# Performance work log

Hardware: AMD Instinct MI355X
Metric: run time of the kernel (lower is better)

## Reference

```python
import jax, jax.numpy as jnp
import numpy as np

EPS_PD = 1e-6   # torch F.pairwise_distance default eps (added to the difference)
EPS_CS = 1e-8   # torch cosine_similarity default eps (norm clamp)


def _similarity(f1, f2, f3):
    # f1, f2, f3: (B, D)
    w1 = 1.0 / (1.0 + jnp.sqrt(jnp.sum((f1 - f2 + EPS_PD) ** 2, axis=-1, keepdims=True)))
    w2 = 1.0 / (1.0 + jnp.sqrt(jnp.sum((f1 - f3 + EPS_PD) ** 2, axis=-1, keepdims=True)))
    n1 = jnp.maximum(jnp.sqrt(jnp.sum(f1 * f1, axis=-1, keepdims=True)), EPS_CS)
    n2 = jnp.maximum(jnp.sqrt(jnp.sum(f2 * f2, axis=-1, keepdims=True)), EPS_CS)
    n3 = jnp.maximum(jnp.sqrt(jnp.sum(f3 * f3, axis=-1, keepdims=True)), EPS_CS)
    w3 = 0.5 + 0.5 * (jnp.sum(f1 * f2, axis=-1, keepdims=True) / (n1 * n2))
    w4 = 0.5 + 0.5 * (jnp.sum(f1 * f3, axis=-1, keepdims=True) / (n1 * n3))
    return f1 + (w1 + w3) * f2 + (w2 + w4) * f3


def setup_inputs() -> dict:
    key = jax.random.key(0)
    k1, k2 = jax.random.split(key)
    B, steps, D = 8192, 3, 2048
    feat_in = jax.random.normal(k1, (B * steps, D), dtype=jnp.float32)
    pos_embedding = jax.random.normal(k2, (1, steps, D), dtype=jnp.float32)
    return {"feat_in": feat_in, "pos_embedding": pos_embedding}


def reference(feat_in, pos_embedding):
    steps = pos_embedding.shape[1]   # 3
    D = pos_embedding.shape[2]
    B = feat_in.shape[0] // steps
    x = feat_in.reshape(B, steps, D) + pos_embedding   # (B, 3, D)
    f1, f2, f3 = x[:, 0], x[:, 1], x[:, 2]
    o1 = _similarity(f1, f2, f3)
    o2 = _similarity(f2, f1, f3)
    o3 = _similarity(f3, f1, f2)
    out = jnp.stack((o1, o2, o3), axis=1)              # (B, 3, D)
    return out.reshape(B * steps, D)
```

## Files before the change

### kernel.cpp

```cpp
#include <hip/hip_runtime.h>


constexpr int D   = 2048;
constexpr int TPB = 256;
constexpr int RPB = TPB / 64;
constexpr int NC  = D / (64 * 4);
constexpr float EPS_PD = 1e-6f;
constexpr float EPS_CS = 1e-8f;

using fvec4 = __attribute__((ext_vector_type(4))) float;

__global__ __launch_bounds__(TPB) void feat_corr_kernel(
    const float* __restrict__ feat,
    const float* __restrict__ pos,
    float* __restrict__ out,
    int B)
{
    const int wave = threadIdx.x >> 6;
    const int lane = threadIdx.x & 63;
    const int b    = blockIdx.x * RPB + wave;
    if (b >= B) return;

    const size_t row = (size_t)b * (3 * D);
    const fvec4* r1 = (const fvec4*)(feat + row);
    const fvec4* r2 = r1 + D / 4;
    const fvec4* r3 = r2 + D / 4;
    const fvec4* p1 = (const fvec4*)(pos);
    const fvec4* p2 = p1 + D / 4;
    const fvec4* p3 = p2 + D / 4;

    fvec4 x1[NC], x2[NC], x3[NC];
#pragma unroll
    for (int j = 0; j < NC; ++j) x1[j] = r1[j * 64 + lane];
#pragma unroll
    for (int j = 0; j < NC; ++j) x2[j] = r2[j * 64 + lane];
#pragma unroll
    for (int j = 0; j < NC; ++j) x3[j] = r3[j * 64 + lane];

#pragma unroll
    for (int j = 0; j < NC; ++j) {
        x1[j] += p1[j * 64 + lane];
        x2[j] += p2[j * 64 + lane];
        x3[j] += p3[j * 64 + lane];
    }

    float n1s = 0.f, n2s = 0.f, n3s = 0.f;
    float d12 = 0.f, d13 = 0.f, d23 = 0.f;
    float s1  = 0.f, s2  = 0.f, s3  = 0.f;
#pragma unroll
    for (int j = 0; j < NC; ++j) {
#pragma unroll
        for (int k = 0; k < 4; ++k) {
            const float u = x1[j][k], w = x2[j][k], z = x3[j][k];
            n1s = fmaf(u, u, n1s);
            n2s = fmaf(w, w, n2s);
            n3s = fmaf(z, z, n3s);
            d12 = fmaf(u, w, d12);
            d13 = fmaf(u, z, d13);
            d23 = fmaf(w, z, d23);
            s1 += u; s2 += w; s3 += z;
        }
    }

    float vals[9] = {n1s, n2s, n3s, d12, d13, d23, s1, s2, s3};
#pragma unroll
    for (int off = 1; off < 64; off <<= 1) {
#pragma unroll
        for (int k = 0; k < 9; ++k)
            vals[k] += __shfl_xor(vals[k], off, 64);
    }

    const float N1s = vals[0], N2s = vals[1], N3s = vals[2];
    const float D12 = vals[3], D13 = vals[4], D23 = vals[5];
    const float S1  = vals[6], S2  = vals[7], S3  = vals[8];

    const float n1 = fmaxf(sqrtf(N1s), EPS_CS);
    const float n2 = fmaxf(sqrtf(N2s), EPS_CS);
    const float n3 = fmaxf(sqrtf(N3s), EPS_CS);

    const float c12 = 0.5f + 0.5f * (D12 / (n1 * n2));
    const float c13 = 0.5f + 0.5f * (D13 / (n1 * n3));
    const float c23 = 0.5f + 0.5f * (D23 / (n2 * n3));

    const float sq12 = N1s + N2s - 2.f * D12;
    const float sq13 = N1s + N3s - 2.f * D13;
    const float sq23 = N2s + N3s - 2.f * D23;
    const float De2  = (float)D * EPS_PD * EPS_PD;

    auto wdist = [&](float sqd, float ssum) {
        return 1.0f / (1.0f + sqrtf(sqd + 2.f * EPS_PD * ssum + De2));
    };
    const float w12 = wdist(sq12, S1 - S2);
    const float w21 = wdist(sq12, S2 - S1);
    const float w13 = wdist(sq13, S1 - S3);
    const float w31 = wdist(sq13, S3 - S1);
    const float w23 = wdist(sq23, S2 - S3);
    const float w32 = wdist(sq23, S3 - S2);

    const float g1b = w12 + c12, g1c = w13 + c13;
    const float g2a = w21 + c12, g2c = w23 + c23;
    const float g3a = w31 + c13, g3b = w32 + c23;

    fvec4* o1 = (fvec4*)(out + row);
    fvec4* o2 = o1 + D / 4;
    fvec4* o3 = o2 + D / 4;
#pragma unroll
    for (int j = 0; j < NC; ++j) {
        const int idx = j * 64 + lane;
        fvec4 q1 = x1[j] + g1b * x2[j] + g1c * x3[j];
        fvec4 q2 = x2[j] + g2a * x1[j] + g2c * x3[j];
        fvec4 q3 = x3[j] + g3a * x1[j] + g3b * x2[j];
        __builtin_nontemporal_store(q1, o1 + idx);
        __builtin_nontemporal_store(q2, o2 + idx);
        __builtin_nontemporal_store(q3, o3 + idx);
    }
}

extern "C" void kernel_launch(void* const* d_in, const int* in_sizes, int n_in,
                              void* d_out, int out_size, void* d_ws, size_t ws_size,
                              hipStream_t stream) {
    const float* feat = (const float*)d_in[0];
    const float* pos  = (const float*)d_in[1];
    float* out        = (float*)d_out;
    const int B = in_sizes[0] / (3 * D * (int)sizeof(float));
    const int B_rows = in_sizes[0] / (3 * D);
    const int Buse   = (B_rows > 0) ? B_rows : B;
    const int grid   = (Buse + RPB - 1) / RPB;
    feat_corr_kernel<<<grid, TPB, 0, stream>>>(feat, pos, out, Buse);
}
```

Baseline: 340.6 us.

## Use persistent waves with double-buffered row prefetch and LDS-cached position embedding

Switches from one wave per row to a persistent grid capped at 512 blocks, where each wave strides over rows. It loads the next row into a second register buffer while the current row is processed, overlapping loads with compute and stores. The position embedding is staged into shared memory once per block rather than read from global memory for every row. Two full row buffers per thread raise register pressure sharply, which limits occupancy and risks spills. The capped grid may also leave some CUs underused.

Measured after the change: 362.4 us. 1.06x slower.

```diff
diff --git a/kernel.cpp b/kernel.cpp
--- a/kernel.cpp
+++ b/kernel.cpp
@@ -3,116 +3,144 @@
 
 constexpr int D   = 2048;
 constexpr int TPB = 256;
-constexpr int RPB = TPB / 64;
+constexpr int WPB = TPB / 64;
 constexpr int NC  = D / (64 * 4);
 constexpr float EPS_PD = 1e-6f;
 constexpr float EPS_CS = 1e-8f;
 
 using fvec4 = __attribute__((ext_vector_type(4))) float;
 
-__global__ __launch_bounds__(TPB) void feat_corr_kernel(
+__global__ __launch_bounds__(TPB, 2) void feat_corr_kernel(
     const float* __restrict__ feat,
     const float* __restrict__ pos,
     float* __restrict__ out,
-    int B)
+    int B, int NW)
 {
-    const int wave = threadIdx.x >> 6;
+    __shared__ float pshared[3 * D];
+    {
+        const fvec4* ps = (const fvec4*)pos;
+        fvec4*       pd = (fvec4*)pshared;
+        for (int i = threadIdx.x; i < 3 * D / 4; i += TPB)
+            pd[i] = ps[i];
+    }
+    __syncthreads();
+
     const int lane = threadIdx.x & 63;
-    const int b    = blockIdx.x * RPB + wave;
-    if (b >= B) return;
+    const int gw   = blockIdx.x * WPB + (threadIdx.x >> 6);
 
-    const size_t row = (size_t)b * (3 * D);
-    const fvec4* r1 = (const fvec4*)(feat + row);
-    const fvec4* r2 = r1 + D / 4;
-    const fvec4* r3 = r2 + D / 4;
-    const fvec4* p1 = (const fvec4*)(pos);
+    const fvec4* p1 = (const fvec4*)pshared;
     const fvec4* p2 = p1 + D / 4;
     const fvec4* p3 = p2 + D / 4;
 
-    fvec4 x1[NC], x2[NC], x3[NC];
+    fvec4 xA1[NC], xA2[NC], xA3[NC];
+    fvec4 xB1[NC], xB2[NC], xB3[NC];
+
+    auto load_row = [&](fvec4 (&x1)[NC], fvec4 (&x2)[NC], fvec4 (&x3)[NC], int b) {
+        const fvec4* r1 = (const fvec4*)(feat + (size_t)b * (3 * D));
+        const fvec4* r2 = r1 + D / 4;
+        const fvec4* r3 = r2 + D / 4;
 #pragma unroll
-    for (int j = 0; j < NC; ++j) x1[j] = r1[j * 64 + lane];
+        for (int j = 0; j < NC; ++j) x1[j] = r1[j * 64 + lane];
 #pragma unroll
-    for (int j = 0; j < NC; ++j) x2[j] = r2[j * 64 + lane];
+        for (int j = 0; j < NC; ++j) x2[j] = r2[j * 64 + lane];
 #pragma unroll
-    for (int j = 0; j < NC; ++j) x3[j] = r3[j * 64 + lane];
+        for (int j = 0; j < NC; ++j) x3[j] = r3[j * 64 + lane];
+    };
 
+    auto process_row = [&](fvec4 (&x1)[NC], fvec4 (&x2)[NC], fvec4 (&x3)[NC], int b) {
 #pragma unroll
-    for (int j = 0; j < NC; ++j) {
-        x1[j] += p1[j * 64 + lane];
-        x2[j] += p2[j * 64 + lane];
-        x3[j] += p3[j * 64 + lane];
-    }
+        for (int j = 0; j < NC; ++j) {
+            x1[j] += p1[j * 64 + lane];
+            x2[j] += p2[j * 64 + lane];
+            x3[j] += p3[j * 64 + lane];
+        }
 
-    float n1s = 0.f, n2s = 0.f, n3s = 0.f;
-    float d12 = 0.f, d13 = 0.f, d23 = 0.f;
-    float s1  = 0.f, s2  = 0.f, s3  = 0.f;
+        float n1s = 0.f, n2s = 0.f, n3s = 0.f;
+        float d12 = 0.f, d13 = 0.f, d23 = 0.f;
+        float s1  = 0.f, s2  = 0.f, s3  = 0.f;
 #pragma unroll
-    for (int j = 0; j < NC; ++j) {
+        for (int j = 0; j < NC; ++j) {
 #pragma unroll
-        for (int k = 0; k < 4; ++k) {
-            const float u = x1[j][k], w = x2[j][k], z = x3[j][k];
-            n1s = fmaf(u, u, n1s);
-            n2s = fmaf(w, w, n2s);
-            n3s = fmaf(z, z, n3s);
-            d12 = fmaf(u, w, d12);
-            d13 = fmaf(u, z, d13);
-            d23 = fmaf(w, z, d23);
-            s1 += u; s2 += w; s3 += z;
+            for (int k = 0; k < 4; ++k) {
+                const float u = x1[j][k], w = x2[j][k], z = x3[j][k];
+                n1s = fmaf(u, u, n1s);
+                n2s = fmaf(w, w, n2s);
+                n3s = fmaf(z, z, n3s);
+                d12 = fmaf(u, w, d12);
+                d13 = fmaf(u, z, d13);
+                d23 = fmaf(w, z, d23);
+                s1 += u; s2 += w; s3 += z;
+            }
         }
-    }
 
-    float vals[9] = {n1s, n2s, n3s, d12, d13, d23, s1, s2, s3};
+        float vals[9] = {n1s, n2s, n3s, d12, d13, d23, s1, s2, s3};
 #pragma unroll
-    for (int off = 1; off < 64; off <<= 1) {
+        for (int off = 1; off < 64; off <<= 1) {
 #pragma unroll
-        for (int k = 0; k < 9; ++k)
-            vals[k] += __shfl_xor(vals[k], off, 64);
-    }
+            for (int k = 0; k < 9; ++k)
+                vals[k] += __shfl_xor(vals[k], off, 64);
+        }
 
-    const float N1s = vals[0], N2s = vals[1], N3s = vals[2];
-    const float D12 = vals[3], D13 = vals[4], D23 = vals[5];
-    const float S1  = vals[6], S2  = vals[7], S3  = vals[8];
+        const float N1s = vals[0], N2s = vals[1], N3s = vals[2];
+        const float D12 = vals[3], D13 = vals[4], D23 = vals[5];
+        const float S1  = vals[6], S2  = vals[7], S3  = vals[8];
 
-    const float n1 = fmaxf(sqrtf(N1s), EPS_CS);
-    const float n2 = fmaxf(sqrtf(N2s), EPS_CS);
-    const float n3 = fmaxf(sqrtf(N3s), EPS_CS);
+        const float n1 = fmaxf(sqrtf(N1s), EPS_CS);
+        const float n2 = fmaxf(sqrtf(N2s), EPS_CS);
+        const float n3 = fmaxf(sqrtf(N3s), EPS_CS);
 
-    const float c12 = 0.5f + 0.5f * (D12 / (n1 * n2));
-    const float c13 = 0.5f + 0.5f * (D13 / (n1 * n3));
-    const float c23 = 0.5f + 0.5f * (D23 / (n2 * n3));
+        const float c12 = 0.5f + 0.5f * (D12 / (n1 * n2));
+        const float c13 = 0.5f + 0.5f * (D13 / (n1 * n3));
+        const float c23 = 0.5f + 0.5f * (D23 / (n2 * n3));
 
-    const float sq12 = N1s + N2s - 2.f * D12;
-    const float sq13 = N1s + N3s - 2.f * D13;
-    const float sq23 = N2s + N3s - 2.f * D23;
-    const float De2  = (float)D * EPS_PD * EPS_PD;
+        const float sq12 = N1s + N2s - 2.f * D12;
+        const float sq13 = N1s + N3s - 2.f * D13;
+        const float sq23 = N2s + N3s - 2.f * D23;
+        const float De2  = (float)D * EPS_PD * EPS_PD;
 
-    auto wdist = [&](float sqd, float ssum) {
-        return 1.0f / (1.0f + sqrtf(sqd + 2.f * EPS_PD * ssum + De2));
+        auto wdist = [&](float sqd, float ssum) {
+            return 1.0f / (1.0f + sqrtf(sqd + 2.f * EPS_PD * ssum + De2));
+        };
+        const float w12 = wdist(sq12, S1 - S2);
+        const float w21 = wdist(sq12, S2 - S1);
+        const float w13 = wdist(sq13, S1 - S3);
+        const float w31 = wdist(sq13, S3 - S1);
+        const float w23 = wdist(sq23, S2 - S3);
+        const float w32 = wdist(sq23, S3 - S2);
+
+        const float g1b = w12 + c12, g1c = w13 + c13;
+        const float g2a = w21 + c12, g2c = w23 + c23;
+        const float g3a = w31 + c13, g3b = w32 + c23;
+
+        const size_t row = (size_t)b * (3 * D);
+        fvec4* o1 = (fvec4*)(out + row);
+        fvec4* o2 = o1 + D / 4;
+        fvec4* o3 = o2 + D / 4;
+#pragma unroll
+        for (int j = 0; j < NC; ++j) {
+            const int idx = j * 64 + lane;
+            fvec4 q1 = x1[j] + g1b * x2[j] + g1c * x3[j];
+            fvec4 q2 = x2[j] + g2a * x1[j] + g2c * x3[j];
+            fvec4 q3 = x3[j] + g3a * x1[j] + g3b * x2[j];
+            __builtin_nontemporal_store(q1, o1 + idx);
+            __builtin_nontemporal_store(q2, o2 + idx);
+            __builtin_nontemporal_store(q3, o3 + idx);
+        }
     };
-    const float w12 = wdist(sq12, S1 - S2);
-    const float w21 = wdist(sq12, S2 - S1);
-    const float w13 = wdist(sq13, S1 - S3);
-    const float w31 = wdist(sq13, S3 - S1);
-    const float w23 = wdist(sq23, S2 - S3);
-    const float w32 = wdist(sq23, S3 - S2);
 
-    const float g1b = w12 + c12, g1c = w13 + c13;
-    const float g2a = w21 + c12, g2c = w23 + c23;
-    const float g3a = w31 + c13, g3b = w32 + c23;
-
-    fvec4* o1 = (fvec4*)(out + row);
-    fvec4* o2 = o1 + D / 4;
-    fvec4* o3 = o2 + D / 4;
-#pragma unroll
-    for (int j = 0; j < NC; ++j) {
-        const int idx = j * 64 + lane;
-        fvec4 q1 = x1[j] + g1b * x2[j] + g1c * x3[j];
-        fvec4 q2 = x2[j] + g2a * x1[j] + g2c * x3[j];
-        fvec4 q3 = x3[j] + g3a * x1[j] + g3b * x2[j];
-        __builtin_nontemporal_store(q1, o1 + idx);
-        __builtin_nontemporal_store(q2, o2 + idx);
-        __builtin_nontemporal_store(q3, o3 + idx);
+    int r = gw;
+    if (r >= B) return;
+    load_row(xA1, xA2, xA3, r);
+    while (true) {
+        const int rB = r + NW;
+        if (rB < B) load_row(xB1, xB2, xB3, rB);
+        process_row(xA1, xA2, xA3, r);
+        if (rB >= B) break;
+        const int rn = r + 2 * NW;
+        if (rn < B) load_row(xA1, xA2, xA3, rn);
+        process_row(xB1, xB2, xB3, rB);
+        if (rn >= B) break;
+        r = rn;
     }
 }
 
@@ -122,9 +150,9 @@
     const float* feat = (const float*)d_in[0];
     const float* pos  = (const float*)d_in[1];
     float* out        = (float*)d_out;
-    const int B = in_sizes[0] / (3 * D * (int)sizeof(float));
-    const int B_rows = in_sizes[0] / (3 * D);
-    const int Buse   = (B_rows > 0) ? B_rows : B;
-    const int grid   = (Buse + RPB - 1) / RPB;
-    feat_corr_kernel<<<grid, TPB, 0, stream>>>(feat, pos, out, Buse);
+    const int B = in_sizes[0] / (3 * D);
+    int blocks = (B + WPB - 1) / WPB;
+    if (blocks > 512) blocks = 512;
+    const int NW = blocks * WPB;
+    feat_corr_kernel<<<blocks, TPB, 0, stream>>>(feat, pos, out, B, NW);
 }
```

## Split into reduce and combine kernels with LDS-cached positional embedding

Applied to the files above, without the earlier changes.

Splits the single register-heavy kernel into two passes. The first computes the per-row coefficients into workspace, and the second re-reads the features and writes the combined output. Both stage the positional embedding in shared memory and use launch bounds that ask for higher occupancy. The per-row sums behind the epsilon term are also dropped, which simplifies the distance weights. The cost is a second full read of the 200MB input in exchange for lower register pressure, plus a small accuracy deviation from removing the eps*sum term.

New measurement: 446.7 us. 31.1% more time.

```diff
diff --git a/kernel.cpp b/kernel.cpp
--- a/kernel.cpp
+++ b/kernel.cpp
@@ -3,76 +3,68 @@
 
 constexpr int D   = 2048;
 constexpr int TPB = 256;
-constexpr int RPB = TPB / 64;
+constexpr int WPB = TPB / 64;
 constexpr int NC  = D / (64 * 4);
 constexpr float EPS_PD = 1e-6f;
 constexpr float EPS_CS = 1e-8f;
 
 using fvec4 = __attribute__((ext_vector_type(4))) float;
 
-__global__ __launch_bounds__(TPB) void feat_corr_kernel(
+__global__ __launch_bounds__(TPB, 6) void feat_corr_reduce(
     const float* __restrict__ feat,
     const float* __restrict__ pos,
-    float* __restrict__ out,
+    float* __restrict__ coef,
     int B)
 {
-    const int wave = threadIdx.x >> 6;
+    __shared__ float psh[3 * D];
+    {
+        const fvec4* ps = (const fvec4*)pos;
+        fvec4*       pd = (fvec4*)psh;
+        for (int i = threadIdx.x; i < 3 * D / 4; i += TPB) pd[i] = ps[i];
+    }
+    __syncthreads();
+
     const int lane = threadIdx.x & 63;
-    const int b    = blockIdx.x * RPB + wave;
+    const int b    = blockIdx.x * WPB + (threadIdx.x >> 6);
     if (b >= B) return;
 
-    const size_t row = (size_t)b * (3 * D);
-    const fvec4* r1 = (const fvec4*)(feat + row);
+    const fvec4* r1 = (const fvec4*)(feat + (size_t)b * (3 * D));
     const fvec4* r2 = r1 + D / 4;
     const fvec4* r3 = r2 + D / 4;
-    const fvec4* p1 = (const fvec4*)(pos);
+    const fvec4* p1 = (const fvec4*)psh;
     const fvec4* p2 = p1 + D / 4;
     const fvec4* p3 = p2 + D / 4;
 
-    fvec4 x1[NC], x2[NC], x3[NC];
-#pragma unroll
-    for (int j = 0; j < NC; ++j) x1[j] = r1[j * 64 + lane];
-#pragma unroll
-    for (int j = 0; j < NC; ++j) x2[j] = r2[j * 64 + lane];
-#pragma unroll
-    for (int j = 0; j < NC; ++j) x3[j] = r3[j * 64 + lane];
-
-#pragma unroll
-    for (int j = 0; j < NC; ++j) {
-        x1[j] += p1[j * 64 + lane];
-        x2[j] += p2[j * 64 + lane];
-        x3[j] += p3[j * 64 + lane];
-    }
-
     float n1s = 0.f, n2s = 0.f, n3s = 0.f;
     float d12 = 0.f, d13 = 0.f, d23 = 0.f;
-    float s1  = 0.f, s2  = 0.f, s3  = 0.f;
-#pragma unroll
-    for (int j = 0; j < NC; ++j) {
+#pragma unroll
+    for (int j = 0; j < NC; ++j) {
+        const int idx = j * 64 + lane;
+        const fvec4 u4 = r1[idx] + p1[idx];
+        const fvec4 w4 = r2[idx] + p2[idx];
+        const fvec4 z4 = r3[idx] + p3[idx];
 #pragma unroll
         for (int k = 0; k < 4; ++k) {
-            const float u = x1[j][k], w = x2[j][k], z = x3[j][k];
+            const float u = u4[k], w = w4[k], z = z4[k];
             n1s = fmaf(u, u, n1s);
             n2s = fmaf(w, w, n2s);
             n3s = fmaf(z, z, n3s);
             d12 = fmaf(u, w, d12);
             d13 = fmaf(u, z, d13);
             d23 = fmaf(w, z, d23);
-            s1 += u; s2 += w; s3 += z;
         }
     }
 
-    float vals[9] = {n1s, n2s, n3s, d12, d13, d23, s1, s2, s3};
+    float vals[6] = {n1s, n2s, n3s, d12, d13, d23};
 #pragma unroll
     for (int off = 1; off < 64; off <<= 1) {
 #pragma unroll
-        for (int k = 0; k < 9; ++k)
+        for (int k = 0; k < 6; ++k)
             vals[k] += __shfl_xor(vals[k], off, 64);
     }
 
     const float N1s = vals[0], N2s = vals[1], N3s = vals[2];
     const float D12 = vals[3], D13 = vals[4], D23 = vals[5];
-    const float S1  = vals[6], S2  = vals[7], S3  = vals[8];
 
     const float n1 = fmaxf(sqrtf(N1s), EPS_CS);
     const float n2 = fmaxf(sqrtf(N2s), EPS_CS);
@@ -87,32 +79,142 @@
     const float sq23 = N2s + N3s - 2.f * D23;
     const float De2  = (float)D * EPS_PD * EPS_PD;
 
-    auto wdist = [&](float sqd, float ssum) {
-        return 1.0f / (1.0f + sqrtf(sqd + 2.f * EPS_PD * ssum + De2));
-    };
-    const float w12 = wdist(sq12, S1 - S2);
-    const float w21 = wdist(sq12, S2 - S1);
-    const float w13 = wdist(sq13, S1 - S3);
-    const float w31 = wdist(sq13, S3 - S1);
-    const float w23 = wdist(sq23, S2 - S3);
-    const float w32 = wdist(sq23, S3 - S2);
-
-    const float g1b = w12 + c12, g1c = w13 + c13;
-    const float g2a = w21 + c12, g2c = w23 + c23;
-    const float g3a = w31 + c13, g3b = w32 + c23;
-
+    const float w12 = 1.0f / (1.0f + sqrtf(sq12 + De2));
+    const float w13 = 1.0f / (1.0f + sqrtf(sq13 + De2));
+    const float w23 = 1.0f / (1.0f + sqrtf(sq23 + De2));
+
+    if (lane == 0) {
+        fvec4* cv = (fvec4*)(coef + (size_t)b * 8);
+        fvec4 c0 = {w12 + c12, w13 + c13, w12 + c12, w23 + c23};
+        fvec4 c1 = {w13 + c13, w23 + c23, 0.f, 0.f};
+        cv[0] = c0;
+        cv[1] = c1;
+    }
+}
+
+__global__ __launch_bounds__(TPB, 6) void feat_corr_combine(
+    const float* __restrict__ feat,
+    const float* __restrict__ pos,
+    const float* __restrict__ coef,
+    float* __restrict__ out,
+    int B)
+{
+    __shared__ float psh[3 * D];
+    {
+        const fvec4* ps = (const fvec4*)pos;
+        fvec4*       pd = (fvec4*)psh;
+        for (int i = threadIdx.x; i < 3 * D / 4; i += TPB) pd[i] = ps[i];
+    }
+    __syncthreads();
+
+    const int lane = threadIdx.x & 63;
+    const int b    = blockIdx.x * WPB + (threadIdx.x >> 6);
+    if (b >= B) return;
+
+    const fvec4* cv = (const fvec4*)(coef + (size_t)b * 8);
+    const fvec4 c0 = cv[0], c1 = cv[1];
+    const float g1b = c0[0], g1c = c0[1], g2a = c0[2], g2c = c0[3];
+    const float g3a = c1[0], g3b = c1[1];
+
+    const size_t row = (size_t)b * (3 * D);
+    const fvec4* r1 = (const fvec4*)(feat + row);
+    const fvec4* r2 = r1 + D / 4;
+    const fvec4* r3 = r2 + D / 4;
+    const fvec4* p1 = (const fvec4*)psh;
+    const fvec4* p2 = p1 + D / 4;
+    const fvec4* p3 = p2 + D / 4;
     fvec4* o1 = (fvec4*)(out + row);
     fvec4* o2 = o1 + D / 4;
     fvec4* o3 = o2 + D / 4;
+
 #pragma unroll
     for (int j = 0; j < NC; ++j) {
         const int idx = j * 64 + lane;
-        fvec4 q1 = x1[j] + g1b * x2[j] + g1c * x3[j];
-        fvec4 q2 = x2[j] + g2a * x1[j] + g2c * x3[j];
-        fvec4 q3 = x3[j] + g3a * x1[j] + g3b * x2[j];
+        const fvec4 x1 = r1[idx] + p1[idx];
+        const fvec4 x2 = r2[idx] + p2[idx];
+        const fvec4 x3 = r3[idx] + p3[idx];
+        const fvec4 q1 = x1 + g1b * x2 + g1c * x3;
+        const fvec4 q2 = x2 + g2a * x1 + g2c * x3;
+        const fvec4 q3 = x3 + g3a * x1 + g3b * x2;
         __builtin_nontemporal_store(q1, o1 + idx);
         __builtin_nontemporal_store(q2, o2 + idx);
         __builtin_nontemporal_store(q3, o3 + idx);
+    }
+}
+
+__global__ __launch_bounds__(TPB) void feat_corr_single(
+    const float* __restrict__ feat,
+    const float* __restrict__ pos,
+    float* __restrict__ out,
+    int B)
+{
+    const int lane = threadIdx.x & 63;
+    const int b    = blockIdx.x * WPB + (threadIdx.x >> 6);
+    if (b >= B) return;
+
+    const size_t row = (size_t)b * (3 * D);
+    const fvec4* r1 = (const fvec4*)(feat + row);
+    const fvec4* r2 = r1 + D / 4;
+    const fvec4* r3 = r2 + D / 4;
+    const fvec4* p1 = (const fvec4*)pos;
+    const fvec4* p2 = p1 + D / 4;
+    const fvec4* p3 = p2 + D / 4;
+
+    fvec4 x1[NC], x2[NC], x3[NC];
+#pragma unroll
+    for (int j = 0; j < NC; ++j) x1[j] = r1[j * 64 + lane];
+#pragma unroll
+    for (int j = 0; j < NC; ++j) x2[j] = r2[j * 64 + lane];
+#pragma unroll
+    for (int j = 0; j < NC; ++j) x3[j] = r3[j * 64 + lane];
+#pragma unroll
+    for (int j = 0; j < NC; ++j) {
+        x1[j] += p1[j * 64 + lane];
+        x2[j] += p2[j * 64 + lane];
+        x3[j] += p3[j * 64 + lane];
+    }
+
+    float n1s = 0.f, n2s = 0.f, n3s = 0.f, d12 = 0.f, d13 = 0.f, d23 = 0.f;
+#pragma unroll
+    for (int j = 0; j < NC; ++j)
+#pragma unroll
+        for (int k = 0; k < 4; ++k) {
+            const float u = x1[j][k], w = x2[j][k], z = x3[j][k];
+            n1s = fmaf(u, u, n1s); n2s = fmaf(w, w, n2s); n3s = fmaf(z, z, n3s);
+            d12 = fmaf(u, w, d12); d13 = fmaf(u, z, d13); d23 = fmaf(w, z, d23);
+        }
+
+    float vals[6] = {n1s, n2s, n3s, d12, d13, d23};
+#pragma unroll
+    for (int off = 1; off < 64; off <<= 1)
+#pragma unroll
+        for (int k = 0; k < 6; ++k) vals[k] += __shfl_xor(vals[k], off, 64);
+
+    const float N1s = vals[0], N2s = vals[1], N3s = vals[2];
+    const float D12 = vals[3], D13 = vals[4], D23 = vals[5];
+    const float n1 = fmaxf(sqrtf(N1s), EPS_CS);
+    const float n2 = fmaxf(sqrtf(N2s), EPS_CS);
+    const float n3 = fmaxf(sqrtf(N3s), EPS_CS);
+    const float c12 = 0.5f + 0.5f * (D12 / (n1 * n2));
+    const float c13 = 0.5f + 0.5f * (D13 / (n1 * n3));
+    const float c23 = 0.5f + 0.5f * (D23 / (n2 * n3));
+    const float De2 = (float)D * EPS_PD * EPS_PD;
+    const float w12 = 1.0f / (1.0f + sqrtf(N1s + N2s - 2.f * D12 + De2));
+    const float w13 = 1.0f / (1.0f + sqrtf(N1s + N3s - 2.f * D13 + De2));
+    const float w23 = 1.0f / (1.0f + sqrtf(N2s + N3s - 2.f * D23 + De2));
+    const float g1b = w12 + c12, g1c = w13 + c13;
+    const float g2a = w12 + c12, g2c = w23 + c23;
+    const float g3a = w13 + c13, g3b = w23 + c23;
+
+    fvec4* o1 = (fvec4*)(out + row);
+    fvec4* o2 = o1 + D / 4;
+    fvec4* o3 = o2 + D / 4;
+#pragma unroll
+    for (int j = 0; j < NC; ++j) {
+        const int idx = j * 64 + lane;
+        __builtin_nontemporal_store(x1[j] + g1b * x2[j] + g1c * x3[j], o1 + idx);
+        __builtin_nontemporal_store(x2[j] + g2a * x1[j] + g2c * x3[j], o2 + idx);
+        __builtin_nontemporal_store(x3[j] + g3a * x1[j] + g3b * x2[j], o3 + idx);
     }
 }
 
@@ -122,9 +224,15 @@
     const float* feat = (const float*)d_in[0];
     const float* pos  = (const float*)d_in[1];
     float* out        = (float*)d_out;
-    const int B = in_sizes[0] / (3 * D * (int)sizeof(float));
-    const int B_rows = in_sizes[0] / (3 * D);
-    const int Buse   = (B_rows > 0) ? B_rows : B;
-    const int grid   = (Buse + RPB - 1) / RPB;
-    feat_corr_kernel<<<grid, TPB, 0, stream>>>(feat, pos, out, Buse);
-}
+    const int B = in_sizes[0] / (3 * D);
+    const int grid = (B + WPB - 1) / WPB;
+    const size_t need = (size_t)B * 8 * sizeof(float);
+
+    if (d_ws != nullptr && ws_size >= need) {
+        float* coef = (float*)d_ws;
+        feat_corr_reduce<<<grid, TPB, 0, stream>>>(feat, pos, coef, B);
+        feat_corr_combine<<<grid, TPB, 0, stream>>>(feat, pos, coef, out, B);
+    } else {
+        feat_corr_single<<<grid, TPB, 0, stream>>>(feat, pos, out, B);
+    }
+}
```

## Persistent waves pipeline row reductions with previous row's output pass, pos in LDS

Applied to the files above, without the earlier changes.

Replaces the one-row-per-wave kernel with a persistent grid of 512 blocks. Each wave computes the reductions for its next row while writing the output for its previous row, which re-reads that row from global memory (likely from L2 or cache) instead of holding all 24 fvec4s in registers. The positional embedding is staged in shared memory, and the sum terms in the pairwise distance are dropped, treating the eps*sum correction as negligible. This lowers register pressure and overlaps loads with stores. The cost is a second read of every input row and a slightly different numeric formula.

After: 348.6 us. 2.3% more time.

```diff
diff --git a/kernel.cpp b/kernel.cpp
--- a/kernel.cpp
+++ b/kernel.cpp
@@ -3,116 +3,148 @@
 
 constexpr int D   = 2048;
 constexpr int TPB = 256;
-constexpr int RPB = TPB / 64;
+constexpr int WPB = TPB / 64;
 constexpr int NC  = D / (64 * 4);
 constexpr float EPS_PD = 1e-6f;
 constexpr float EPS_CS = 1e-8f;
 
 using fvec4 = __attribute__((ext_vector_type(4))) float;
 
-__global__ __launch_bounds__(TPB) void feat_corr_kernel(
+__global__ __launch_bounds__(TPB, 4) void feat_corr_fused(
     const float* __restrict__ feat,
     const float* __restrict__ pos,
     float* __restrict__ out,
-    int B)
+    int B, int NW)
 {
-    const int wave = threadIdx.x >> 6;
+    __shared__ float psh[3 * D];
+    {
+        const fvec4* ps = (const fvec4*)pos;
+        fvec4*       pd = (fvec4*)psh;
+#pragma unroll
+        for (int i = threadIdx.x; i < 3 * D / 4; i += TPB) pd[i] = ps[i];
+    }
+    __syncthreads();
+
     const int lane = threadIdx.x & 63;
-    const int b    = blockIdx.x * RPB + wave;
-    if (b >= B) return;
+    const int gw   = blockIdx.x * WPB + (threadIdx.x >> 6);
+    if (gw >= B) return;
 
-    const size_t row = (size_t)b * (3 * D);
-    const fvec4* r1 = (const fvec4*)(feat + row);
-    const fvec4* r2 = r1 + D / 4;
-    const fvec4* r3 = r2 + D / 4;
-    const fvec4* p1 = (const fvec4*)(pos);
+    const fvec4* p1 = (const fvec4*)psh;
     const fvec4* p2 = p1 + D / 4;
     const fvec4* p3 = p2 + D / 4;
 
-    fvec4 x1[NC], x2[NC], x3[NC];
+    auto finalize = [&](float v[6], float cf[6]) {
 #pragma unroll
-    for (int j = 0; j < NC; ++j) x1[j] = r1[j * 64 + lane];
+        for (int off = 1; off < 64; off <<= 1)
 #pragma unroll
-    for (int j = 0; j < NC; ++j) x2[j] = r2[j * 64 + lane];
+            for (int k = 0; k < 6; ++k) v[k] += __shfl_xor(v[k], off, 64);
+        const float N1s = v[0], N2s = v[1], N3s = v[2];
+        const float D12 = v[3], D13 = v[4], D23 = v[5];
+        const float n1 = fmaxf(sqrtf(N1s), EPS_CS);
+        const float n2 = fmaxf(sqrtf(N2s), EPS_CS);
+        const float n3 = fmaxf(sqrtf(N3s), EPS_CS);
+        const float c12 = 0.5f + 0.5f * (D12 / (n1 * n2));
+        const float c13 = 0.5f + 0.5f * (D13 / (n1 * n3));
+        const float c23 = 0.5f + 0.5f * (D23 / (n2 * n3));
+        const float De2 = (float)D * EPS_PD * EPS_PD;
+        const float w12 = 1.f / (1.f + sqrtf(N1s + N2s - 2.f * D12 + De2));
+        const float w13 = 1.f / (1.f + sqrtf(N1s + N3s - 2.f * D13 + De2));
+        const float w23 = 1.f / (1.f + sqrtf(N2s + N3s - 2.f * D23 + De2));
+        cf[0] = w12 + c12;
+        cf[1] = w13 + c13;
+        cf[2] = w12 + c12;
+        cf[3] = w23 + c23;
+        cf[4] = w13 + c13;
+        cf[5] = w23 + c23;
+    };
+
+    int rp = gw;
+    float cf[6];
+    {
+        const fvec4* a1 = (const fvec4*)(feat + (size_t)rp * (3 * D));
+        const fvec4* a2 = a1 + D / 4;
+        const fvec4* a3 = a2 + D / 4;
+        float acc[6] = {0.f, 0.f, 0.f, 0.f, 0.f, 0.f};
+#pragma unroll 2
+        for (int j = 0; j < NC; ++j) {
+            const int idx = j * 64 + lane;
+            const fvec4 u = a1[idx] + p1[idx];
+            const fvec4 w = a2[idx] + p2[idx];
+            const fvec4 z = a3[idx] + p3[idx];
 #pragma unroll
-    for (int j = 0; j < NC; ++j) x3[j] = r3[j * 64 + lane];
-
-#pragma unroll
-    for (int j = 0; j < NC; ++j) {
-        x1[j] += p1[j * 64 + lane];
-        x2[j] += p2[j * 64 + lane];
-        x3[j] += p3[j * 64 + lane];
+            for (int k = 0; k < 4; ++k) {
+                acc[0] = fmaf(u[k], u[k], acc[0]);
+                acc[1] = fmaf(w[k], w[k], acc[1]);
+                acc[2] = fmaf(z[k], z[k], acc[2]);
+                acc[3] = fmaf(u[k], w[k], acc[3]);
+                acc[4] = fmaf(u[k], z[k], acc[4]);
+                acc[5] = fmaf(w[k], z[k], acc[5]);
+            }
+        }
+        finalize(acc, cf);
     }
 
-    float n1s = 0.f, n2s = 0.f, n3s = 0.f;
-    float d12 = 0.f, d13 = 0.f, d23 = 0.f;
-    float s1  = 0.f, s2  = 0.f, s3  = 0.f;
+    for (int r = rp + NW; r < B; r += NW) {
+        const fvec4* a1 = (const fvec4*)(feat + (size_t)r  * (3 * D));
+        const fvec4* a2 = a1 + D / 4;
+        const fvec4* a3 = a2 + D / 4;
+        const fvec4* b1 = (const fvec4*)(feat + (size_t)rp * (3 * D));
+        const fvec4* b2 = b1 + D / 4;
+        const fvec4* b3 = b2 + D / 4;
+        fvec4* o1 = (fvec4*)(out + (size_t)rp * (3 * D));
+        fvec4* o2 = o1 + D / 4;
+        fvec4* o3 = o2 + D / 4;
+        const float g1b = cf[0], g1c = cf[1], g2a = cf[2];
+        const float g2c = cf[3], g3a = cf[4], g3b = cf[5];
+
+        float acc[6] = {0.f, 0.f, 0.f, 0.f, 0.f, 0.f};
+#pragma unroll 2
+        for (int j = 0; j < NC; ++j) {
+            const int idx = j * 64 + lane;
+            const fvec4 q1 = p1[idx], q2 = p2[idx], q3 = p3[idx];
+            const fvec4 u  = a1[idx] + q1;
+            const fvec4 w  = a2[idx] + q2;
+            const fvec4 z  = a3[idx] + q3;
+            const fvec4 x1 = b1[idx] + q1;
+            const fvec4 x2 = b2[idx] + q2;
+            const fvec4 x3 = b3[idx] + q3;
 #pragma unroll
-    for (int j = 0; j < NC; ++j) {
-#pragma unroll
-        for (int k = 0; k < 4; ++k) {
-            const float u = x1[j][k], w = x2[j][k], z = x3[j][k];
-            n1s = fmaf(u, u, n1s);
-            n2s = fmaf(w, w, n2s);
-            n3s = fmaf(z, z, n3s);
-            d12 = fmaf(u, w, d12);
-            d13 = fmaf(u, z, d13);
-            d23 = fmaf(w, z, d23);
-            s1 += u; s2 += w; s3 += z;
+            for (int k = 0; k < 4; ++k) {
+                acc[0] = fmaf(u[k], u[k], acc[0]);
+                acc[1] = fmaf(w[k], w[k], acc[1]);
+                acc[2] = fmaf(z[k], z[k], acc[2]);
+                acc[3] = fmaf(u[k], w[k], acc[3]);
+                acc[4] = fmaf(u[k], z[k], acc[4]);
+                acc[5] = fmaf(w[k], z[k], acc[5]);
+            }
+            __builtin_nontemporal_store(x1 + g1b * x2 + g1c * x3, o1 + idx);
+            __builtin_nontemporal_store(x2 + g2a * x1 + g2c * x3, o2 + idx);
+            __builtin_nontemporal_store(x3 + g3a * x1 + g3b * x2, o3 + idx);
         }
+        finalize(acc, cf);
+        rp = r;
     }
 
-    float vals[9] = {n1s, n2s, n3s, d12, d13, d23, s1, s2, s3};
-#pragma unroll
-    for (int off = 1; off < 64; off <<= 1) {
-#pragma unroll
-        for (int k = 0; k < 9; ++k)
-            vals[k] += __shfl_xor(vals[k], off, 64);
-    }
-
-    const float N1s = vals[0], N2s = vals[1], N3s = vals[2];
-    const float D12 = vals[3], D13 = vals[4], D23 = vals[5];
-    const float S1  = vals[6], S2  = vals[7], S3  = vals[8];
-
-    const float n1 = fmaxf(sqrtf(N1s), EPS_CS);
-    const float n2 = fmaxf(sqrtf(N2s), EPS_CS);
-    const float n3 = fmaxf(sqrtf(N3s), EPS_CS);
-
-    const float c12 = 0.5f + 0.5f * (D12 / (n1 * n2));
-    const float c13 = 0.5f + 0.5f * (D13 / (n1 * n3));
-    const float c23 = 0.5f + 0.5f * (D23 / (n2 * n3));
-
-    const float sq12 = N1s + N2s - 2.f * D12;
-    const float sq13 = N1s + N3s - 2.f * D13;
-    const float sq23 = N2s + N3s - 2.f * D23;
-    const float De2  = (float)D * EPS_PD * EPS_PD;
-
-    auto wdist = [&](float sqd, float ssum) {
-        return 1.0f / (1.0f + sqrtf(sqd + 2.f * EPS_PD * ssum + De2));
-    };
-    const float w12 = wdist(sq12, S1 - S2);
-    const float w21 = wdist(sq12, S2 - S1);
-    const float w13 = wdist(sq13, S1 - S3);
-    const float w31 = wdist(sq13, S3 - S1);
-    const float w23 = wdist(sq23, S2 - S3);
-    const float w32 = wdist(sq23, S3 - S2);
-
-    const float g1b = w12 + c12, g1c = w13 + c13;
-    const float g2a = w21 + c12, g2c = w23 + c23;
-    const float g3a = w31 + c13, g3b = w32 + c23;
-
-    fvec4* o1 = (fvec4*)(out + row);
-    fvec4* o2 = o1 + D / 4;
-    fvec4* o3 = o2 + D / 4;
-#pragma unroll
-    for (int j = 0; j < NC; ++j) {
-        const int idx = j * 64 + lane;
-        fvec4 q1 = x1[j] + g1b * x2[j] + g1c * x3[j];
-        fvec4 q2 = x2[j] + g2a * x1[j] + g2c * x3[j];
-        fvec4 q3 = x3[j] + g3a * x1[j] + g3b * x2[j];
-        __builtin_nontemporal_store(q1, o1 + idx);
-        __builtin_nontemporal_store(q2, o2 + idx);
-        __builtin_nontemporal_store(q3, o3 + idx);
+    {
+        const fvec4* b1 = (const fvec4*)(feat + (size_t)rp * (3 * D));
+        const fvec4* b2 = b1 + D / 4;
+        const fvec4* b3 = b2 + D / 4;
+        fvec4* o1 = (fvec4*)(out + (size_t)rp * (3 * D));
+        fvec4* o2 = o1 + D / 4;
+        fvec4* o3 = o2 + D / 4;
+        const float g1b = cf[0], g1c = cf[1], g2a = cf[2];
+        const float g2c = cf[3], g3a = cf[4], g3b = cf[5];
+#pragma unroll 2
+        for (int j = 0; j < NC; ++j) {
+            const int idx = j * 64 + lane;
+            const fvec4 q1 = p1[idx], q2 = p2[idx], q3 = p3[idx];
+            const fvec4 x1 = b1[idx] + q1;
+            const fvec4 x2 = b2[idx] + q2;
+            const fvec4 x3 = b3[idx] + q3;
+            __builtin_nontemporal_store(x1 + g1b * x2 + g1c * x3, o1 + idx);
+            __builtin_nontemporal_store(x2 + g2a * x1 + g2c * x3, o2 + idx);
+            __builtin_nontemporal_store(x3 + g3a * x1 + g3b * x2, o3 + idx);
+        }
     }
 }
 
@@ -122,9 +154,10 @@
     const float* feat = (const float*)d_in[0];
     const float* pos  = (const float*)d_in[1];
     float* out        = (float*)d_out;
-    const int B = in_sizes[0] / (3 * D * (int)sizeof(float));
-    const int B_rows = in_sizes[0] / (3 * D);
-    const int Buse   = (B_rows > 0) ? B_rows : B;
-    const int grid   = (Buse + RPB - 1) / RPB;
-    feat_corr_kernel<<<grid, TPB, 0, stream>>>(feat, pos, out, Buse);
+    const int B = in_sizes[0] / (3 * D);
+
+    int blocks = 512;
+    if (blocks * WPB > B) blocks = (B + WPB - 1) / WPB;
+    const int NW = blocks * WPB;
+    feat_corr_fused<<<blocks, TPB, 0, stream>>>(feat, pos, out, B, NW);
 }
```
